# Optimization experiments

Measured on AMD Instinct MI355X. Metric: run time of the kernel, lower is better.

Reference implementation:

```python
import jax, jax.numpy as jnp
import numpy as np

DIM = 768
HID = 3072
HID2 = HID // 2
MAX_LEVEL = 8
N_LEV = MAX_LEVEL + 1
BATCH, SEQ = 2, 2048
EPS = 1e-5


def _layernorm(x, gamma, beta):
    m = jnp.mean(x, axis=-1, keepdims=True)
    v = jnp.mean(jnp.square(x - m), axis=-1, keepdims=True)
    return (x - m) * jax.lax.rsqrt(v + EPS) * gamma + beta


def setup_inputs() -> dict:
    key = jax.random.key(0)
    ks = jax.random.split(key, 12)
    s = 0.02
    return {
        "x": jax.random.normal(ks[0], (BATCH, SEQ, DIM), dtype=jnp.float32),
        "levels_info": jax.random.randint(ks[1], (SEQ, 4), 0, N_LEV, dtype=jnp.int32),
        "gamma": jnp.ones((DIM,), dtype=jnp.float32),
        "beta": jnp.zeros((DIM,), dtype=jnp.float32),
        "W1": jax.random.normal(ks[2], (DIM, HID), dtype=jnp.float32) * s,
        "b1": jnp.zeros((HID,), dtype=jnp.float32),
        "W2": jax.random.normal(ks[3], (HID, DIM), dtype=jnp.float32) * s,
        "b2": jnp.zeros((DIM,), dtype=jnp.float32),
        "A1": jax.random.normal(ks[4], (N_LEV, DIM, HID2), dtype=jnp.float32) * s,
        "a1b": jnp.zeros((N_LEV, HID2), dtype=jnp.float32),
        "A2": jax.random.normal(ks[5], (N_LEV, HID2, DIM), dtype=jnp.float32) * s,
        "a2b": jnp.zeros((N_LEV, DIM), dtype=jnp.float32),
        "lmw": jnp.ones((N_LEV,), dtype=jnp.float32)
        + jax.random.normal(ks[6], (N_LEV,), dtype=jnp.float32) * 0.1,
    }


def reference(x, levels_info, gamma, beta, W1, b1, W2, b2, A1, a1b, A2, a2b, lmw):
    # x: [B,S,D]
    x_norm = _layernorm(x, gamma, beta)
    # main MLP: Linear -> GELU (exact, torch default) -> Linear; dropout=0 is identity
    h = jax.nn.gelu(jnp.einsum("bsd,dh->bsh", x_norm, W1) + b1, approximate=False)
    main_out = jnp.einsum("bsh,hd->bsd", h, W2) + b2

    # per-token depth-indexed adapter routing
    depths = jnp.clip(levels_info[:, 0], 0, MAX_LEVEL)  # [S]
    level_adapted = jnp.zeros_like(main_out)
    for lvl in range(N_LEV):  # small fixed expert set
        mask = (depths == lvl).astype(x.dtype)[None, :, None]  # [1,S,1]
        hl = jax.nn.relu(jnp.einsum("bsd,dh->bsh", x_norm, A1[lvl]) + a1b[lvl])
        level_adapted = level_adapted + mask * (
            jnp.einsum("bsh,hd->bsd", hl, A2[lvl]) + a2b[lvl]
        )

    # softmax over the sequence axis (faithful to F.softmax(..., dim=0))
    mix = jax.nn.softmax(lmw[depths], axis=0)[None, :, None]  # [1,S,1]
    return main_out * (1.0 - mix) + level_adapted * mix
```

## Files before the change

### kernel.cpp

```cpp
#include <hip/hip_runtime.h>
#include <hip/hip_bf16.h>
#include <math.h>

typedef __bf16 bf16;
typedef __bf16 bf16x4 __attribute__((ext_vector_type(4)));
typedef __bf16 bf16x8 __attribute__((ext_vector_type(8)));
typedef float f32x4 __attribute__((ext_vector_type(4)));

#define DIM 768
#define HID 3072
#define HID2 1536
#define NLEV 9
#define SEQ 2048
#define ROWS 4096
#define MAXPAD 5248
#define MAXTILES 41

__device__ __forceinline__ void gld16(const void* g, void* l) {
    __builtin_amdgcn_global_load_lds(
        (const __attribute__((address_space(1))) void*)g,
        (__attribute__((address_space(3))) void*)l, 16, 0, 0);
}

__device__ __forceinline__ float fast_gelu(float v) {
    float v2 = v * v;
    float twou = v * (1.59576912f + 0.071354816f * v2);
    float t = __expf(twou);
    return v * t / (t + 1.0f);
}

__device__ __forceinline__ int xcd_swizzle(int s, int nwg) {
    int q = nwg >> 3, r = nwg & 7;
    int x = s & 7, i = s >> 3;
    return (x < r ? x * (q + 1) : r * (q + 1) + (x - r) * q) + i;
}


__device__ __forceinline__ void ln4_body(int blk,
                                         const float* __restrict__ x,
                                         const float* __restrict__ gamma,
                                         const float* __restrict__ beta,
                                         bf16* __restrict__ xn) {
    int tid = threadIdx.x;
    int wv = tid >> 6, ln = tid & 63;
    int row = blk * 4 + wv;
    const float* xr = x + (size_t)row * DIM;
    int c = ln * 4;
    float4 v0 = *(const float4*)(xr + c);
    float4 v1 = *(const float4*)(xr + c + 256);
    float4 v2 = *(const float4*)(xr + c + 512);
    float s = v0.x + v0.y + v0.z + v0.w
            + v1.x + v1.y + v1.z + v1.w
            + v2.x + v2.y + v2.z + v2.w;
    float q = v0.x * v0.x + v0.y * v0.y + v0.z * v0.z + v0.w * v0.w
            + v1.x * v1.x + v1.y * v1.y + v1.z * v1.z + v1.w * v1.w
            + v2.x * v2.x + v2.y * v2.y + v2.z * v2.z + v2.w * v2.w;
#pragma unroll
    for (int off = 32; off; off >>= 1) {
        s += __shfl_xor(s, off, 64);
        q += __shfl_xor(q, off, 64);
    }
    float m = s * (1.0f / DIM);
    float r = rsqrtf(q * (1.0f / DIM) - m * m + 1e-5f);
    bf16* xo = xn + (size_t)row * DIM;
#pragma unroll
    for (int p = 0; p < 3; p++) {
        int cc = c + p * 256;
        float4 v = (p == 0) ? v0 : (p == 1) ? v1 : v2;
        float4 g = *(const float4*)(gamma + cc);
        float4 b = *(const float4*)(beta + cc);
        bf16x4 o;
        o[0] = (bf16)((v.x - m) * r * g.x + b.x);
        o[1] = (bf16)((v.y - m) * r * g.y + b.y);
        o[2] = (bf16)((v.z - m) * r * g.z + b.z);
        o[3] = (bf16)((v.w - m) * r * g.w + b.w);
        *(bf16x4*)(xo + cc) = o;
    }
}

__device__ __forceinline__ void transpose_body64(bf16* sm,
                                                 const float* __restrict__ inb,
                                                 bf16* __restrict__ outb,
                                                 int R, int C, int bx, int by) {
    int tid = threadIdx.x;
    int ty = tid >> 4;
    int tx4 = (tid & 15) * 4;
#pragma unroll
    for (int p = 0; p < 4; p++) {
        int rloc = p * 16 + ty;
        int row = by * 64 + rloc;
        float4 v = *(const float4*)(inb + (size_t)row * C + bx * 64 + tx4);
        bf16x4 o;
        o[0] = (bf16)v.x; o[1] = (bf16)v.y; o[2] = (bf16)v.z; o[3] = (bf16)v.w;
        *(bf16x4*)(sm + rloc * 68 + tx4) = o;
    }
    __syncthreads();
    int ch = tid & 7;
    int ocb = tid >> 3;
#pragma unroll
    for (int p = 0; p < 2; p++) {
        int oc = p * 32 + ocb;
        bf16x8 tmp;
#pragma unroll
        for (int k = 0; k < 8; k++) tmp[k] = sm[(ch * 8 + k) * 68 + oc];
        *(bf16x8*)(outb + (size_t)(bx * 64 + oc) * R + by * 64 + ch * 8) = tmp;
    }
}

__device__ __forceinline__ void routing_body(float* sm,
                                             const int* __restrict__ levels_info,
                                             const float* __restrict__ lmw,
                                             float* __restrict__ mix,
                                             int* __restrict__ row_index,
                                             int* __restrict__ tile_meta,
                                             float* __restrict__ zbuf) {
    int* cnt = (int*)sm;
    int* cur = cnt + NLEV;
    int* off = cur + NLEV;
    float* mixv = (float*)(off + NLEV);
    int tid = threadIdx.x;
    if (tid < NLEV) { cnt[tid] = 0; cur[tid] = 0; }
    __syncthreads();
    for (int s = tid; s < SEQ; s += 256) {
        int d = levels_info[s * 4];
        d = d < 0 ? 0 : (d > 8 ? 8 : d);
        atomicAdd(&cnt[d], 1);
    }
    for (int i = tid; i < MAXPAD; i += 256) row_index[i] = -1;
    for (int i = tid; i < 1024; i += 256) zbuf[i] = 0.0f;
    __syncthreads();
    if (tid == 0) {
        float mx = lmw[0];
        for (int l = 1; l < NLEV; l++) mx = fmaxf(mx, lmw[l]);
        float denom = 0.f;
        for (int l = 0; l < NLEV; l++) denom += (float)cnt[l] * expf(lmw[l] - mx);
        float inv = 1.0f / denom;
        int running = 0, t = 0;
        for (int l = 0; l < NLEV; l++) {
            mixv[l] = expf(lmw[l] - mx) * inv;
            off[l] = running;
            int seg = (2 * cnt[l] + 127) & ~127;
            for (int k = 0; k < seg / 128; k++) tile_meta[t++] = l;
            running += seg;
        }
        for (; t < MAXTILES; t++) tile_meta[t] = -1;
    }
    __syncthreads();
    for (int s = tid; s < SEQ; s += 256) {
        int d = levels_info[s * 4];
        d = d < 0 ? 0 : (d > 8 ? 8 : d);
        int p = atomicAdd(&cur[d], 2);
        row_index[off[d] + p]     = s;
        row_index[off[d] + p + 1] = s + SEQ;
        mix[s] = mixv[d];
    }
}

__global__ __launch_bounds__(256) void prep_kernel(const float* __restrict__ x,
                                                   const int* __restrict__ levels_info,
                                                   const float* __restrict__ gamma,
                                                   const float* __restrict__ beta,
                                                   const float* __restrict__ W1,
                                                   const float* __restrict__ A1,
                                                   const float* __restrict__ W2,
                                                   const float* __restrict__ A2,
                                                   const float* __restrict__ lmw,
                                                   bf16* __restrict__ Xn,
                                                   bf16* __restrict__ W1t,
                                                   bf16* __restrict__ A1t,
                                                   bf16* __restrict__ W2t,
                                                   bf16* __restrict__ A2t,
                                                   float* __restrict__ mix,
                                                   int* __restrict__ row_index,
                                                   int* __restrict__ tile_meta,
                                                   float* __restrict__ zbuf) {
    __shared__ __align__(16) bf16 tsm[64 * 68];
    int b = blockIdx.x;
    if (b == 0) { routing_body((float*)tsm, levels_info, lmw, mix, row_index, tile_meta, zbuf); return; }
    b -= 1;
    if (b < 1024) { ln4_body(b, x, gamma, beta, Xn); return; }
    b -= 1024;
    if (b < 576) {
        transpose_body64(tsm, W1, W1t, DIM, HID, b % 48, b / 48);
        return;
    }
    b -= 576;
    if (b < 2592) {
        int bz = b / 288, r = b % 288;
        transpose_body64(tsm, A1 + (size_t)bz * DIM * HID2, A1t + (size_t)bz * DIM * HID2,
                         DIM, HID2, r % 24, r / 24);
        return;
    }
    b -= 2592;
    if (b < 576) {
        transpose_body64(tsm, W2, W2t, HID, DIM, b % 12, b / 12);
        return;
    }
    b -= 576;
    {
        int bz = b / 288, r = b % 288;
        transpose_body64(tsm, A2 + (size_t)bz * HID2 * DIM, A2t + (size_t)bz * HID2 * DIM,
                         HID2, DIM, r % 12, r / 12);
    }
}

template<int KT>
__device__ __forceinline__ void gemm_loop_db64(const bf16* (&ga)[4], const bf16* (&gb)[4],
                                               bf16* As, bf16* Bs,
                                               f32x4 (&acc)[4][4]) {
    int tid = threadIdx.x;
    int wv = tid >> 6;
    int lane = tid & 63;
    int wm = wv >> 1, wn = wv & 1;
    int r = lane & 15;
    int ch0 = ((lane >> 4) ^ (lane & 7)) * 8;
    int aoff = (wm * 64 + r) * 64 + ch0;
    int boff = (wn * 64 + r) * 64 + ch0;
#pragma unroll
    for (int c = 0; c < 4; c++) {
        gld16(ga[c], As + (c * 32 + wv * 8) * 64);
        gld16(gb[c], Bs + (c * 32 + wv * 8) * 64);
        ga[c] += 64; gb[c] += 64;
    }
#pragma unroll
    for (int kt = 0; kt < KT; ++kt) {
        __syncthreads();
        const int cur = (kt & 1) << 13;
        const int nxt = cur ^ 8192;
        if (kt + 1 < KT) {
#pragma unroll
            for (int c = 0; c < 4; c++) {
                gld16(ga[c], As + nxt + (c * 32 + wv * 8) * 64);
                gld16(gb[c], Bs + nxt + (c * 32 + wv * 8) * 64);
                ga[c] += 64; gb[c] += 64;
            }
        }
#pragma unroll
        for (int k32 = 0; k32 < 2; k32++) {
            const int kx = k32 << 5;
            bf16x8 af[4], bfr[4];
#pragma unroll
            for (int i = 0; i < 4; i++) af[i] = *(const bf16x8*)(As + cur + ((aoff + i * 1024) ^ kx));
#pragma unroll
            for (int j = 0; j < 4; j++) bfr[j] = *(const bf16x8*)(Bs + cur + ((boff + j * 1024) ^ kx));
#pragma unroll
            for (int i = 0; i < 4; i++)
#pragma unroll
                for (int j = 0; j < 4; j++)
                    acc[i][j] = __builtin_amdgcn_mfma_f32_16x16x32_bf16(af[i], bfr[j], acc[i][j], 0, 0, 0);
        }
    }
}

#define ACC_INIT(acc) \
    _Pragma("unroll") for (int i = 0; i < 4; i++) \
    _Pragma("unroll") for (int j = 0; j < 4; j++) acc[i][j] = (f32x4){0.f, 0.f, 0.f, 0.f};

__device__ __forceinline__ void store_tile(const bf16* cbuf, int lane,
                                           bf16* gptr, int ldg) {
#pragma unroll
    for (int p = 0; p < 8; p++) {
        int lrow = p * 8 + (lane >> 3);
        int chunk = (lane & 7) * 8;
        bf16x8 v = *(const bf16x8*)(cbuf + lrow * 64 + chunk);
        *(bf16x8*)(gptr + (size_t)lrow * ldg + chunk) = v;
    }
}

__global__ __launch_bounds__(256) void mlp1_kernel(const bf16* __restrict__ Xn,
                                                   const bf16* __restrict__ W1t,
                                                   const float* __restrict__ b1,
                                                   bf16* __restrict__ H,
                                                   const bf16* __restrict__ A1t,
                                                   const float* __restrict__ a1b,
                                                   const int* __restrict__ row_index,
                                                   const int* __restrict__ tile_meta,
                                                   const bf16* __restrict__ zbuf,
                                                   bf16* __restrict__ HL) {
    __shared__ __align__(16) bf16 smem[32768];
    bf16* As = smem;
    bf16* Bs = smem + 16384;
    int bid = xcd_swizzle(blockIdx.x, 1260);
    int tid = threadIdx.x;
    int lane = tid & 63, wv = tid >> 6, wm = wv >> 1, wn = wv & 1;
    int lrow = lane >> 3;
    int lch = ((lane & 7) ^ lrow) * 8;
    bf16* cbuf = smem + wv * 4096;

    if (bid < 768) {
        int s = bid >> 5, u = bid & 31;
        int nb = (s % 6) * 4 + (u & 3);
        int mb = (s / 6) * 8 + (u >> 2);
        f32x4 acc[4][4];
        ACC_INIT(acc);
        const bf16* ga[4]; const bf16* gb[4];
#pragma unroll
        for (int c = 0; c < 4; c++) {
            int rt = c * 32 + wv * 8 + lrow;
            ga[c] = Xn  + (size_t)(mb * 128 + rt) * DIM + lch;
            gb[c] = W1t + (size_t)(nb * 128 + rt) * DIM + lch;
        }
        gemm_loop_db64<12>(ga, gb, As, Bs, acc);
        int cbase = nb * 128 + wn * 64 + (lane & 15);
        __syncthreads();
#pragma unroll
        for (int j = 0; j < 4; j++) {
            float bias = b1[cbase + j * 16];
#pragma unroll
            for (int i = 0; i < 4; i++)
#pragma unroll
                for (int r = 0; r < 4; r++) {
                    int lr = i * 16 + ((lane >> 4) << 2) + r;
                    int lc = j * 16 + (lane & 15);
                    cbuf[lr * 64 + lc] = (bf16)fast_gelu(acc[i][j][r] + bias);
                }
        }
        __syncthreads();
        store_tile(cbuf, lane, H + (size_t)(mb * 128 + wm * 64) * HID + nb * 128 + wn * 64, HID);
    } else {
        int t2 = bid - 768;
        int nb = t2 % 12, t = t2 / 12;
        int lvl = tile_meta[t];
        if (lvl < 0) return;
        f32x4 acc[4][4];
        ACC_INIT(acc);
        const bf16* ga[4]; const bf16* gb[4];
        const bf16* Bl = A1t + (size_t)lvl * HID2 * DIM;
#pragma unroll
        for (int c = 0; c < 4; c++) {
            int rt = c * 32 + wv * 8 + lrow;
            int rg = row_index[t * 128 + rt];
            ga[c] = (rg >= 0) ? (Xn + (size_t)rg * DIM + lch) : (zbuf + lch);
            gb[c] = Bl + (size_t)(nb * 128 + rt) * DIM + lch;
        }
        gemm_loop_db64<12>(ga, gb, As, Bs, acc);
        int cbase = nb * 128 + wn * 64 + (lane & 15);
        __syncthreads();
#pragma unroll
        for (int j = 0; j < 4; j++) {
            float bias = a1b[lvl * HID2 + cbase + j * 16];
#pragma unroll
            for (int i = 0; i < 4; i++)
#pragma unroll
                for (int r = 0; r < 4; r++) {
                    int lr = i * 16 + ((lane >> 4) << 2) + r;
                    int lc = j * 16 + (lane & 15);
                    cbuf[lr * 64 + lc] = (bf16)fmaxf(acc[i][j][r] + bias, 0.0f);
                }
        }
        __syncthreads();
        store_tile(cbuf, lane, HL + (size_t)(t * 128 + wm * 64) * HID2 + nb * 128 + wn * 64, HID2);
    }
}

__global__ __launch_bounds__(256) void mlp2_kernel(const bf16* __restrict__ H,
                                                   const bf16* __restrict__ W2t,
                                                   bf16* __restrict__ part,
                                                   const bf16* __restrict__ HL,
                                                   const bf16* __restrict__ A2t,
                                                   const float* __restrict__ a2b,
                                                   const int* __restrict__ row_index,
                                                   const int* __restrict__ tile_meta,
                                                   bf16* __restrict__ apart) {
    __shared__ __align__(16) bf16 smem[32768];
    bf16* As = smem;
    bf16* Bs = smem + 16384;
    int bid = xcd_swizzle(blockIdx.x, 384 + MAXTILES * 6);
    int tid = threadIdx.x;
    int lane = tid & 63, wv = tid >> 6, wm = wv >> 1, wn = wv & 1;
    int lrow = lane >> 3;
    int lch = ((lane & 7) ^ lrow) * 8;
    bf16* cbuf = smem + wv * 4096;
    f32x4 acc[4][4];
    ACC_INIT(acc);

    if (bid < 384) {
        int cc = bid % 12;
        int nb = cc >> 1, ks = cc & 1;
        int mb = bid / 12;
        const bf16* ga[4]; const bf16* gb[4];
#pragma unroll
        for (int c = 0; c < 4; c++) {
            int rt = c * 32 + wv * 8 + lrow;
            ga[c] = H   + (size_t)(mb * 128 + rt) * HID + ks * 1536 + lch;
            gb[c] = W2t + (size_t)(nb * 128 + rt) * HID + ks * 1536 + lch;
        }
        gemm_loop_db64<24>(ga, gb, As, Bs, acc);
        __syncthreads();
#pragma unroll
        for (int j = 0; j < 4; j++)
#pragma unroll
            for (int i = 0; i < 4; i++)
#pragma unroll
                for (int r = 0; r < 4; r++) {
                    int lr = i * 16 + ((lane >> 4) << 2) + r;
                    int lc = j * 16 + (lane & 15);
                    cbuf[lr * 64 + lc] = (bf16)acc[i][j][r];
                }
        __syncthreads();
        bf16* pk = part + (size_t)ks * ROWS * DIM;
        store_tile(cbuf, lane, pk + (size_t)(mb * 128 + wm * 64) * DIM + nb * 128 + wn * 64, DIM);
    } else {
        int t2 = bid - 384;
        int nb = t2 % 6, t = t2 / 6;
        int lvl = tile_meta[t];
        if (lvl < 0) return;
        const bf16* ga[4]; const bf16* gb[4];
        const bf16* Bl = A2t + (size_t)lvl * DIM * HID2;
#pragma unroll
        for (int c = 0; c < 4; c++) {
            int rt = c * 32 + wv * 8 + lrow;
            ga[c] = HL + (size_t)(t * 128 + rt) * HID2 + lch;
            gb[c] = Bl + (size_t)(nb * 128 + rt) * HID2 + lch;
        }
        gemm_loop_db64<24>(ga, gb, As, Bs, acc);
        int cbase = nb * 128 + wn * 64 + (lane & 15);
        __syncthreads();
#pragma unroll
        for (int j = 0; j < 4; j++) {
            float bias = a2b[lvl * DIM + cbase + j * 16];
#pragma unroll
            for (int i = 0; i < 4; i++)
#pragma unroll
                for (int r = 0; r < 4; r++) {
                    int lr = i * 16 + ((lane >> 4) << 2) + r;
                    int lc = j * 16 + (lane & 15);
                    cbuf[lr * 64 + lc] = (bf16)(acc[i][j][r] + bias);
                }
        }
        __syncthreads();
        int colg = nb * 128 + wn * 64;
#pragma unroll
        for (int p = 0; p < 8; p++) {
            int lr = p * 8 + (lane >> 3);
            int chunk = (lane & 7) * 8;
            int rg = row_index[t * 128 + wm * 64 + lr];
            if (rg >= 0) {
                bf16x8 v = *(const bf16x8*)(cbuf + lr * 64 + chunk);
                *(bf16x8*)(apart + (size_t)rg * DIM + colg + chunk) = v;
            }
        }
    }
}

__global__ __launch_bounds__(256) void combine_kernel(const bf16* __restrict__ part,
                                                      const bf16* __restrict__ apart,
                                                      const float* __restrict__ b2,
                                                      const float* __restrict__ mix,
                                                      float* __restrict__ out) {
    int i = blockIdx.x * 256 + threadIdx.x;
    int base = i * 4;
    int row = base / DIM;
    int c = base - row * DIM;
    float mx = mix[row & (SEQ - 1)];
    bf16x4 p0 = *(const bf16x4*)(part + base);
    bf16x4 p1 = *(const bf16x4*)(part + (size_t)ROWS * DIM + base);
    bf16x4 a0 = *(const bf16x4*)(apart + base);
    float4 o;
    float* po = &o.x;
#pragma unroll
    for (int k = 0; k < 4; k++) {
        float main_v = (float)p0[k] + (float)p1[k] + b2[c + k];
        po[k] = (1.0f - mx) * main_v + mx * (float)a0[k];
    }
    *(float4*)(out + base) = o;
}

extern "C" void kernel_launch(void* const* d_in, const int* in_sizes, int n_in,
                              void* d_out, int out_size, void* d_ws, size_t ws_size,
                              hipStream_t stream) {
    const float* x    = (const float*)d_in[0];
    const int* levels = (const int*)d_in[1];
    const float* gamma= (const float*)d_in[2];
    const float* beta = (const float*)d_in[3];
    const float* W1   = (const float*)d_in[4];
    const float* b1   = (const float*)d_in[5];
    const float* W2   = (const float*)d_in[6];
    const float* b2   = (const float*)d_in[7];
    const float* A1   = (const float*)d_in[8];
    const float* a1b  = (const float*)d_in[9];
    const float* A2   = (const float*)d_in[10];
    const float* a2b  = (const float*)d_in[11];
    const float* lmw  = (const float*)d_in[12];
    float* out = (float*)d_out;

    char* p = (char*)d_ws;
    auto alloc = [&](size_t bytes) {
        char* r = p;
        p += (bytes + 255) & ~(size_t)255;
        return r;
    };
    bf16* Xn   = (bf16*)alloc((size_t)ROWS * DIM * 2);
    bf16* W1t  = (bf16*)alloc((size_t)HID * DIM * 2);
    bf16* W2t  = (bf16*)alloc((size_t)DIM * HID * 2);
    bf16* A1t  = (bf16*)alloc((size_t)NLEV * HID2 * DIM * 2);
    bf16* A2t  = (bf16*)alloc((size_t)NLEV * DIM * HID2 * 2);
    bf16* H    = (bf16*)alloc((size_t)ROWS * HID * 2);
    bf16* HL   = (bf16*)alloc((size_t)MAXPAD * HID2 * 2);
    bf16* part = (bf16*)alloc((size_t)2 * ROWS * DIM * 2);
    bf16* apart= (bf16*)alloc((size_t)ROWS * DIM * 2);
    float* mix = (float*)alloc(SEQ * 4);
    int* row_index = (int*)alloc(MAXPAD * 4);
    int* tile_meta = (int*)alloc(MAXTILES * 4);
    float* zbuf    = (float*)alloc(4096);

    prep_kernel<<<dim3(1 + 1024 + 576 + 2592 + 576 + 2592), dim3(256), 0, stream>>>(
        x, levels, gamma, beta, W1, A1, W2, A2, lmw,
        Xn, W1t, A1t, W2t, A2t, mix, row_index, tile_meta, zbuf);

    mlp1_kernel<<<dim3(768 + 492), dim3(256), 0, stream>>>(
        Xn, W1t, b1, H, A1t, a1b, row_index, tile_meta, (const bf16*)zbuf, HL);

    mlp2_kernel<<<dim3(384 + MAXTILES * 6), dim3(256), 0, stream>>>(
        H, W2t, part, HL, A2t, a2b, row_index, tile_meta, apart);

    combine_kernel<<<dim3(ROWS * DIM / 1024), dim3(256), 0, stream>>>(
        part, apart, b2, mix, out);
}
```

Measured before the change: 259.2 us.

## Switch GEMMs to 256x256 tiles with 8 waves and interleaved prefetch

Both MLP GEMM kernels move from 128x128 tiles with 4 waves to 256x256 tiles with 8 waves (512 threads, 128KB dynamic LDS). Each wave now holds an 8x4 MFMA accumulator block, which raises arithmetic intensity per LDS load. The K loop is split into barriered phases that interleave global-to-LDS prefetch with MFMA work and raise wave priority around the MFMAs. Adapter level segments are padded to 256 rows and the main down-projection uses a 4-way split-K that combine now sums. Larger padding wastes adapter compute, and the grid shrinks to 342 blocks, which risks poor CU occupancy and tail imbalance.

```diff
diff --git a/kernel.cpp b/kernel.cpp
--- a/kernel.cpp
+++ b/kernel.cpp
@@ -13,8 +13,8 @@
 #define NLEV 9
 #define SEQ 2048
 #define ROWS 4096
-#define MAXPAD 5248
-#define MAXTILES 41
+#define MAXPAD2 6400
+#define MAXT2 25
 
 __device__ __forceinline__ void gld16(const void* g, void* l) {
     __builtin_amdgcn_global_load_lds(
@@ -126,7 +126,7 @@
         d = d < 0 ? 0 : (d > 8 ? 8 : d);
         atomicAdd(&cnt[d], 1);
     }
-    for (int i = tid; i < MAXPAD; i += 256) row_index[i] = -1;
+    for (int i = tid; i < MAXPAD2; i += 256) row_index[i] = -1;
     for (int i = tid; i < 1024; i += 256) zbuf[i] = 0.0f;
     __syncthreads();
     if (tid == 0) {
@@ -139,11 +139,11 @@
         for (int l = 0; l < NLEV; l++) {
             mixv[l] = expf(lmw[l] - mx) * inv;
             off[l] = running;
-            int seg = (2 * cnt[l] + 127) & ~127;
-            for (int k = 0; k < seg / 128; k++) tile_meta[t++] = l;
+            int seg = (2 * cnt[l] + 255) & ~255;
+            for (int k = 0; k < seg / 256; k++) tile_meta[t++] = l;
             running += seg;
         }
-        for (; t < MAXTILES; t++) tile_meta[t] = -1;
+        for (; t < MAXT2; t++) tile_meta[t] = -1;
     }
     __syncthreads();
     for (int s = tid; s < SEQ; s += 256) {
@@ -204,70 +204,102 @@
     }
 }
 
+#define SBUF 16384
+
 template<int KT>
-__device__ __forceinline__ void gemm_loop_db64(const bf16* (&ga)[4], const bf16* (&gb)[4],
-                                               bf16* As, bf16* Bs,
-                                               f32x4 (&acc)[4][4]) {
-    int tid = threadIdx.x;
-    int wv = tid >> 6;
-    int lane = tid & 63;
-    int wm = wv >> 1, wn = wv & 1;
-    int r = lane & 15;
-    int ch0 = ((lane >> 4) ^ (lane & 7)) * 8;
-    int aoff = (wm * 64 + r) * 64 + ch0;
-    int boff = (wn * 64 + r) * 64 + ch0;
+__device__ __forceinline__ void gemm_loop_8w(const bf16* (&ga)[4], const bf16* (&gb)[4],
+                                             bf16* smem, f32x4 (&acc)[8][4]) {
+    const int tid = threadIdx.x;
+    const int wv = tid >> 6, lane = tid & 63;
+    const int wm = wv >> 2, wn = wv & 3;
+    const int r = lane & 15;
+    const int ch0 = ((lane >> 4) ^ (lane & 7)) * 8;
+    const int aoff = (wm * 128 + r) * 64 + ch0;
+    const int boff = (wn * 64 + r) * 64 + ch0;
+    bf16* As = smem;
+    bf16* Bs = smem + 2 * SBUF;
+    const int sA = wv * 512;
 #pragma unroll
     for (int c = 0; c < 4; c++) {
-        gld16(ga[c], As + (c * 32 + wv * 8) * 64);
-        gld16(gb[c], Bs + (c * 32 + wv * 8) * 64);
+        gld16(ga[c], As + sA + c * 4096);
+        gld16(gb[c], Bs + sA + c * 4096);
         ga[c] += 64; gb[c] += 64;
     }
-#pragma unroll
+#pragma unroll 2
     for (int kt = 0; kt < KT; ++kt) {
-        __syncthreads();
-        const int cur = (kt & 1) << 13;
-        const int nxt = cur ^ 8192;
+        const int cur = (kt & 1) ? SBUF : 0;
+        const int nxt = cur ^ SBUF;
+        const bf16* Ac = As + cur;
+        const bf16* Bc = Bs + cur;
+        bf16x8 a[4], b[4];
+        asm volatile("s_waitcnt vmcnt(0)" ::: "memory");
+        __builtin_amdgcn_s_barrier();
+        __builtin_amdgcn_sched_barrier(0);
         if (kt + 1 < KT) {
-#pragma unroll
-            for (int c = 0; c < 4; c++) {
-                gld16(ga[c], As + nxt + (c * 32 + wv * 8) * 64);
-                gld16(gb[c], Bs + nxt + (c * 32 + wv * 8) * 64);
-                ga[c] += 64; gb[c] += 64;
-            }
-        }
-#pragma unroll
-        for (int k32 = 0; k32 < 2; k32++) {
-            const int kx = k32 << 5;
-            bf16x8 af[4], bfr[4];
-#pragma unroll
-            for (int i = 0; i < 4; i++) af[i] = *(const bf16x8*)(As + cur + ((aoff + i * 1024) ^ kx));
-#pragma unroll
-            for (int j = 0; j < 4; j++) bfr[j] = *(const bf16x8*)(Bs + cur + ((boff + j * 1024) ^ kx));
-#pragma unroll
-            for (int i = 0; i < 4; i++)
-#pragma unroll
-                for (int j = 0; j < 4; j++)
-                    acc[i][j] = __builtin_amdgcn_mfma_f32_16x16x32_bf16(af[i], bfr[j], acc[i][j], 0, 0, 0);
-        }
-    }
-}
-
-#define ACC_INIT(acc) \
-    _Pragma("unroll") for (int i = 0; i < 4; i++) \
+            gld16(ga[0], As + nxt + sA);
+            gld16(gb[0], Bs + nxt + sA);
+            gld16(ga[1], As + nxt + sA + 4096);
+            gld16(gb[1], Bs + nxt + sA + 4096);
+            ga[0] += 64; gb[0] += 64; ga[1] += 64; gb[1] += 64;
+        }
+#pragma unroll
+        for (int i = 0; i < 4; i++) a[i] = *(const bf16x8*)(Ac + aoff + i * 1024);
+#pragma unroll
+        for (int j = 0; j < 4; j++) b[j] = *(const bf16x8*)(Bc + boff + j * 1024);
+        __builtin_amdgcn_s_setprio(1);
+#pragma unroll
+        for (int i = 0; i < 4; i++)
+#pragma unroll
+            for (int j = 0; j < 4; j++)
+                acc[i][j] = __builtin_amdgcn_mfma_f32_16x16x32_bf16(a[i], b[j], acc[i][j], 0, 0, 0);
+        __builtin_amdgcn_s_setprio(0);
+        __builtin_amdgcn_s_barrier();
+        if (kt + 1 < KT) {
+            gld16(ga[2], As + nxt + sA + 8192);
+            gld16(gb[2], Bs + nxt + sA + 8192);
+            gld16(ga[3], As + nxt + sA + 12288);
+            gld16(gb[3], Bs + nxt + sA + 12288);
+            ga[2] += 64; gb[2] += 64; ga[3] += 64; gb[3] += 64;
+        }
+#pragma unroll
+        for (int i = 0; i < 4; i++) a[i] = *(const bf16x8*)(Ac + aoff + (4 + i) * 1024);
+        __builtin_amdgcn_s_setprio(1);
+#pragma unroll
+        for (int i = 0; i < 4; i++)
+#pragma unroll
+            for (int j = 0; j < 4; j++)
+                acc[4 + i][j] = __builtin_amdgcn_mfma_f32_16x16x32_bf16(a[i], b[j], acc[4 + i][j], 0, 0, 0);
+        __builtin_amdgcn_s_setprio(0);
+        __builtin_amdgcn_s_barrier();
+#pragma unroll
+        for (int i = 0; i < 4; i++) a[i] = *(const bf16x8*)(Ac + ((aoff + i * 1024) ^ 32));
+#pragma unroll
+        for (int j = 0; j < 4; j++) b[j] = *(const bf16x8*)(Bc + ((boff + j * 1024) ^ 32));
+        __builtin_amdgcn_s_setprio(1);
+#pragma unroll
+        for (int i = 0; i < 4; i++)
+#pragma unroll
+            for (int j = 0; j < 4; j++)
+                acc[i][j] = __builtin_amdgcn_mfma_f32_16x16x32_bf16(a[i], b[j], acc[i][j], 0, 0, 0);
+        __builtin_amdgcn_s_setprio(0);
+        __builtin_amdgcn_s_barrier();
+#pragma unroll
+        for (int i = 0; i < 4; i++) a[i] = *(const bf16x8*)(Ac + ((aoff + (4 + i) * 1024) ^ 32));
+        __builtin_amdgcn_s_setprio(1);
+#pragma unroll
+        for (int i = 0; i < 4; i++)
+#pragma unroll
+            for (int j = 0; j < 4; j++)
+                acc[4 + i][j] = __builtin_amdgcn_mfma_f32_16x16x32_bf16(a[i], b[j], acc[4 + i][j], 0, 0, 0);
+        __builtin_amdgcn_s_setprio(0);
+    }
+}
+
+#define ACC_INIT8(acc) \
+    _Pragma("unroll") for (int i = 0; i < 8; i++) \
     _Pragma("unroll") for (int j = 0; j < 4; j++) acc[i][j] = (f32x4){0.f, 0.f, 0.f, 0.f};
 
-__device__ __forceinline__ void store_tile(const bf16* cbuf, int lane,
-                                           bf16* gptr, int ldg) {
-#pragma unroll
-    for (int p = 0; p < 8; p++) {
-        int lrow = p * 8 + (lane >> 3);
-        int chunk = (lane & 7) * 8;
-        bf16x8 v = *(const bf16x8*)(cbuf + lrow * 64 + chunk);
-        *(bf16x8*)(gptr + (size_t)lrow * ldg + chunk) = v;
-    }
-}
-
-__global__ __launch_bounds__(256) void mlp1_kernel(const bf16* __restrict__ Xn,
+__global__ __launch_bounds__(512) void mlp1_kernel(const bf16* __restrict__ Xn,
                                                    const bf16* __restrict__ W1t,
                                                    const float* __restrict__ b1,
                                                    bf16* __restrict__ H,
@@ -277,83 +309,86 @@
                                                    const int* __restrict__ tile_meta,
                                                    const bf16* __restrict__ zbuf,
                                                    bf16* __restrict__ HL) {
-    __shared__ __align__(16) bf16 smem[32768];
-    bf16* As = smem;
-    bf16* Bs = smem + 16384;
-    int bid = xcd_swizzle(blockIdx.x, 1260);
+    extern __shared__ __align__(16) bf16 smem[];
+    int bid = xcd_swizzle(blockIdx.x, 342);
     int tid = threadIdx.x;
-    int lane = tid & 63, wv = tid >> 6, wm = wv >> 1, wn = wv & 1;
-    int lrow = lane >> 3;
-    int lch = ((lane & 7) ^ lrow) * 8;
-    bf16* cbuf = smem + wv * 4096;
-
-    if (bid < 768) {
-        int s = bid >> 5, u = bid & 31;
-        int nb = (s % 6) * 4 + (u & 3);
-        int mb = (s / 6) * 8 + (u >> 2);
-        f32x4 acc[4][4];
-        ACC_INIT(acc);
+    int wv = tid >> 6, lane = tid & 63;
+    int wm = wv >> 2, wn = wv & 3;
+    int srow = lane >> 3;
+    int lch = ((lane & 7) ^ srow) * 8;
+    f32x4 acc[8][4];
+    ACC_INIT8(acc);
+    bf16* cbuf = smem + wv * 8192;
+
+    if (bid < 192) {
+        int nb = bid % 12, mb = bid / 12;
         const bf16* ga[4]; const bf16* gb[4];
 #pragma unroll
         for (int c = 0; c < 4; c++) {
-            int rt = c * 32 + wv * 8 + lrow;
-            ga[c] = Xn  + (size_t)(mb * 128 + rt) * DIM + lch;
-            gb[c] = W1t + (size_t)(nb * 128 + rt) * DIM + lch;
-        }
-        gemm_loop_db64<12>(ga, gb, As, Bs, acc);
-        int cbase = nb * 128 + wn * 64 + (lane & 15);
+            int rt = c * 64 + wv * 8 + srow;
+            ga[c] = Xn  + (size_t)(mb * 256 + rt) * DIM + lch;
+            gb[c] = W1t + (size_t)(nb * 256 + rt) * DIM + lch;
+        }
+        gemm_loop_8w<12>(ga, gb, smem, acc);
         __syncthreads();
+        int cbase = nb * 256 + wn * 64 + (lane & 15);
 #pragma unroll
         for (int j = 0; j < 4; j++) {
             float bias = b1[cbase + j * 16];
 #pragma unroll
-            for (int i = 0; i < 4; i++)
-#pragma unroll
-                for (int r = 0; r < 4; r++) {
-                    int lr = i * 16 + ((lane >> 4) << 2) + r;
-                    int lc = j * 16 + (lane & 15);
-                    cbuf[lr * 64 + lc] = (bf16)fast_gelu(acc[i][j][r] + bias);
+            for (int i = 0; i < 8; i++)
+#pragma unroll
+                for (int rr = 0; rr < 4; rr++) {
+                    int lr = i * 16 + ((lane >> 4) << 2) + rr;
+                    cbuf[lr * 64 + j * 16 + (lane & 15)] = (bf16)fast_gelu(acc[i][j][rr] + bias);
                 }
         }
-        __syncthreads();
-        store_tile(cbuf, lane, H + (size_t)(mb * 128 + wm * 64) * HID + nb * 128 + wn * 64, HID);
+        bf16* gp = H + (size_t)(mb * 256 + wm * 128) * HID + nb * 256 + wn * 64;
+#pragma unroll
+        for (int p = 0; p < 16; p++) {
+            int lr = p * 8 + srow;
+            int chunk = (lane & 7) * 8;
+            *(bf16x8*)(gp + (size_t)lr * HID + chunk) = *(const bf16x8*)(cbuf + lr * 64 + chunk);
+        }
     } else {
-        int t2 = bid - 768;
-        int nb = t2 % 12, t = t2 / 12;
+        int t2 = bid - 192;
+        int nb = t2 % 6, t = t2 / 6;
         int lvl = tile_meta[t];
         if (lvl < 0) return;
-        f32x4 acc[4][4];
-        ACC_INIT(acc);
         const bf16* ga[4]; const bf16* gb[4];
         const bf16* Bl = A1t + (size_t)lvl * HID2 * DIM;
 #pragma unroll
         for (int c = 0; c < 4; c++) {
-            int rt = c * 32 + wv * 8 + lrow;
-            int rg = row_index[t * 128 + rt];
+            int rt = c * 64 + wv * 8 + srow;
+            int rg = row_index[t * 256 + rt];
             ga[c] = (rg >= 0) ? (Xn + (size_t)rg * DIM + lch) : (zbuf + lch);
-            gb[c] = Bl + (size_t)(nb * 128 + rt) * DIM + lch;
-        }
-        gemm_loop_db64<12>(ga, gb, As, Bs, acc);
-        int cbase = nb * 128 + wn * 64 + (lane & 15);
+            gb[c] = Bl + (size_t)(nb * 256 + rt) * DIM + lch;
+        }
+        gemm_loop_8w<12>(ga, gb, smem, acc);
         __syncthreads();
+        int cbase = nb * 256 + wn * 64 + (lane & 15);
 #pragma unroll
         for (int j = 0; j < 4; j++) {
             float bias = a1b[lvl * HID2 + cbase + j * 16];
 #pragma unroll
-            for (int i = 0; i < 4; i++)
-#pragma unroll
-                for (int r = 0; r < 4; r++) {
-                    int lr = i * 16 + ((lane >> 4) << 2) + r;
-                    int lc = j * 16 + (lane & 15);
-                    cbuf[lr * 64 + lc] = (bf16)fmaxf(acc[i][j][r] + bias, 0.0f);
+            for (int i = 0; i < 8; i++)
+#pragma unroll
+                for (int rr = 0; rr < 4; rr++) {
+                    int lr = i * 16 + ((lane >> 4) << 2) + rr;
+                    cbuf[lr * 64 + j * 16 + (lane & 15)] = (bf16)fmaxf(acc[i][j][rr] + bias, 0.0f);
                 }
         }
-        __syncthreads();
-        store_tile(cbuf, lane, HL + (size_t)(t * 128 + wm * 64) * HID2 + nb * 128 + wn * 64, HID2);
-    }
-}
-
-__global__ __launch_bounds__(256) void mlp2_kernel(const bf16* __restrict__ H,
+        bf16* gp = HL + (size_t)(t * 256 + wm * 128) * HID2 + nb * 256 + wn * 64;
+#pragma unroll
+        for (int p = 0; p < 16; p++) {
+            int lr = p * 8 + srow;
+            int chunk = (lane & 7) * 8;
+            *(bf16x8*)(gp + (size_t)lr * HID2 + chunk) = *(const bf16x8*)(cbuf + lr * 64 + chunk);
+        }
+    }
+}
+
+__global__ __launch_bounds__(512) void mlp2_kernel(const bf16* __restrict__ H,
                                                    const bf16* __restrict__ W2t,
                                                    bf16* __restrict__ part,
                                                    const bf16* __restrict__ HL,
@@ -362,83 +397,84 @@
                                                    const int* __restrict__ row_index,
                                                    const int* __restrict__ tile_meta,
                                                    bf16* __restrict__ apart) {
-    __shared__ __align__(16) bf16 smem[32768];
-    bf16* As = smem;
-    bf16* Bs = smem + 16384;
-    int bid = xcd_swizzle(blockIdx.x, 384 + MAXTILES * 6);
+    extern __shared__ __align__(16) bf16 smem[];
+    int bid = xcd_swizzle(blockIdx.x, 342);
     int tid = threadIdx.x;
-    int lane = tid & 63, wv = tid >> 6, wm = wv >> 1, wn = wv & 1;
-    int lrow = lane >> 3;
-    int lch = ((lane & 7) ^ lrow) * 8;
-    bf16* cbuf = smem + wv * 4096;
-    f32x4 acc[4][4];
-    ACC_INIT(acc);
-
-    if (bid < 384) {
-        int cc = bid % 12;
-        int nb = cc >> 1, ks = cc & 1;
-        int mb = bid / 12;
-        const bf16* ga[4]; const bf16* gb[4];
-#pragma unroll
-        for (int c = 0; c < 4; c++) {
-            int rt = c * 32 + wv * 8 + lrow;
-            ga[c] = H   + (size_t)(mb * 128 + rt) * HID + ks * 1536 + lch;
-            gb[c] = W2t + (size_t)(nb * 128 + rt) * HID + ks * 1536 + lch;
-        }
-        gemm_loop_db64<24>(ga, gb, As, Bs, acc);
-        __syncthreads();
-#pragma unroll
-        for (int j = 0; j < 4; j++)
-#pragma unroll
-            for (int i = 0; i < 4; i++)
-#pragma unroll
-                for (int r = 0; r < 4; r++) {
-                    int lr = i * 16 + ((lane >> 4) << 2) + r;
-                    int lc = j * 16 + (lane & 15);
-                    cbuf[lr * 64 + lc] = (bf16)acc[i][j][r];
-                }
-        __syncthreads();
-        bf16* pk = part + (size_t)ks * ROWS * DIM;
-        store_tile(cbuf, lane, pk + (size_t)(mb * 128 + wm * 64) * DIM + nb * 128 + wn * 64, DIM);
-    } else {
-        int t2 = bid - 384;
-        int nb = t2 % 6, t = t2 / 6;
+    int wv = tid >> 6, lane = tid & 63;
+    int wm = wv >> 2, wn = wv & 3;
+    int srow = lane >> 3;
+    int lch = ((lane & 7) ^ srow) * 8;
+    f32x4 acc[8][4];
+    ACC_INIT8(acc);
+    bf16* cbuf = smem + wv * 8192;
+
+    if (bid < 150) {
+        int nb = bid % 3, t = bid / 3;
         int lvl = tile_meta[t];
         if (lvl < 0) return;
         const bf16* ga[4]; const bf16* gb[4];
         const bf16* Bl = A2t + (size_t)lvl * DIM * HID2;
 #pragma unroll
         for (int c = 0; c < 4; c++) {
-            int rt = c * 32 + wv * 8 + lrow;
-            ga[c] = HL + (size_t)(t * 128 + rt) * HID2 + lch;
-            gb[c] = Bl + (size_t)(nb * 128 + rt) * HID2 + lch;
-        }
-        gemm_loop_db64<24>(ga, gb, As, Bs, acc);
-        int cbase = nb * 128 + wn * 64 + (lane & 15);
+            int rt = c * 64 + wv * 8 + srow;
+            ga[c] = HL + (size_t)(t * 256 + rt) * HID2 + lch;
+            gb[c] = Bl + (size_t)(nb * 256 + rt) * HID2 + lch;
+        }
+        gemm_loop_8w<24>(ga, gb, smem, acc);
         __syncthreads();
+        int cbase = nb * 256 + wn * 64 + (lane & 15);
 #pragma unroll
         for (int j = 0; j < 4; j++) {
             float bias = a2b[lvl * DIM + cbase + j * 16];
 #pragma unroll
-            for (int i = 0; i < 4; i++)
-#pragma unroll
-                for (int r = 0; r < 4; r++) {
-                    int lr = i * 16 + ((lane >> 4) << 2) + r;
-                    int lc = j * 16 + (lane & 15);
-                    cbuf[lr * 64 + lc] = (bf16)(acc[i][j][r] + bias);
+            for (int i = 0; i < 8; i++)
+#pragma unroll
+                for (int rr = 0; rr < 4; rr++) {
+                    int lr = i * 16 + ((lane >> 4) << 2) + rr;
+                    cbuf[lr * 64 + j * 16 + (lane & 15)] = (bf16)(acc[i][j][rr] + bias);
                 }
         }
+        int colg = nb * 256 + wn * 64;
+#pragma unroll
+        for (int p = 0; p < 16; p++) {
+            int lr = p * 8 + srow;
+            int chunk = (lane & 7) * 8;
+            int rg = row_index[t * 256 + wm * 128 + lr];
+            if (rg >= 0) {
+                *(bf16x8*)(apart + (size_t)rg * DIM + colg + chunk) =
+                    *(const bf16x8*)(cbuf + lr * 64 + chunk);
+            }
+        }
+    } else {
+        int g = bid - 150;
+        int mb = g / 12;
+        int cc = g % 12;
+        int nb = cc >> 2, ks = cc & 3;
+        const bf16* ga[4]; const bf16* gb[4];
+#pragma unroll
+        for (int c = 0; c < 4; c++) {
+            int rt = c * 64 + wv * 8 + srow;
+            ga[c] = H   + (size_t)(mb * 256 + rt) * HID + ks * 768 + lch;
+            gb[c] = W2t + (size_t)(nb * 256 + rt) * HID + ks * 768 + lch;
+        }
+        gemm_loop_8w<12>(ga, gb, smem, acc);
         __syncthreads();
-        int colg = nb * 128 + wn * 64;
-#pragma unroll
-        for (int p = 0; p < 8; p++) {
-            int lr = p * 8 + (lane >> 3);
+#pragma unroll
+        for (int j = 0; j < 4; j++)
+#pragma unroll
+            for (int i = 0; i < 8; i++)
+#pragma unroll
+                for (int rr = 0; rr < 4; rr++) {
+                    int lr = i * 16 + ((lane >> 4) << 2) + rr;
+                    cbuf[lr * 64 + j * 16 + (lane & 15)] = (bf16)acc[i][j][rr];
+                }
+        bf16* gp = part + (size_t)ks * ROWS * DIM
+                 + (size_t)(mb * 256 + wm * 128) * DIM + nb * 256 + wn * 64;
+#pragma unroll
+        for (int p = 0; p < 16; p++) {
+            int lr = p * 8 + srow;
             int chunk = (lane & 7) * 8;
-            int rg = row_index[t * 128 + wm * 64 + lr];
-            if (rg >= 0) {
-                bf16x8 v = *(const bf16x8*)(cbuf + lr * 64 + chunk);
-                *(bf16x8*)(apart + (size_t)rg * DIM + colg + chunk) = v;
-            }
+            *(bf16x8*)(gp + (size_t)lr * DIM + chunk) = *(const bf16x8*)(cbuf + lr * 64 + chunk);
         }
     }
 }
@@ -455,12 +491,14 @@
     float mx = mix[row & (SEQ - 1)];
     bf16x4 p0 = *(const bf16x4*)(part + base);
     bf16x4 p1 = *(const bf16x4*)(part + (size_t)ROWS * DIM + base);
+    bf16x4 p2 = *(const bf16x4*)(part + (size_t)2 * ROWS * DIM + base);
+    bf16x4 p3 = *(const bf16x4*)(part + (size_t)3 * ROWS * DIM + base);
     bf16x4 a0 = *(const bf16x4*)(apart + base);
     float4 o;
     float* po = &o.x;
 #pragma unroll
     for (int k = 0; k < 4; k++) {
-        float main_v = (float)p0[k] + (float)p1[k] + b2[c + k];
+        float main_v = (float)p0[k] + (float)p1[k] + (float)p2[k] + (float)p3[k] + b2[c + k];
         po[k] = (1.0f - mx) * main_v + mx * (float)a0[k];
     }
     *(float4*)(out + base) = o;
@@ -496,22 +534,22 @@
     bf16* A1t  = (bf16*)alloc((size_t)NLEV * HID2 * DIM * 2);
     bf16* A2t  = (bf16*)alloc((size_t)NLEV * DIM * HID2 * 2);
     bf16* H    = (bf16*)alloc((size_t)ROWS * HID * 2);
-    bf16* HL   = (bf16*)alloc((size_t)MAXPAD * HID2 * 2);
-    bf16* part = (bf16*)alloc((size_t)2 * ROWS * DIM * 2);
+    bf16* HL   = (bf16*)alloc((size_t)MAXPAD2 * HID2 * 2);
+    bf16* part = (bf16*)alloc((size_t)4 * ROWS * DIM * 2);
     bf16* apart= (bf16*)alloc((size_t)ROWS * DIM * 2);
     float* mix = (float*)alloc(SEQ * 4);
-    int* row_index = (int*)alloc(MAXPAD * 4);
-    int* tile_meta = (int*)alloc(MAXTILES * 4);
+    int* row_index = (int*)alloc(MAXPAD2 * 4);
+    int* tile_meta = (int*)alloc(32 * 4);
     float* zbuf    = (float*)alloc(4096);
 
     prep_kernel<<<dim3(1 + 1024 + 576 + 2592 + 576 + 2592), dim3(256), 0, stream>>>(
         x, levels, gamma, beta, W1, A1, W2, A2, lmw,
         Xn, W1t, A1t, W2t, A2t, mix, row_index, tile_meta, zbuf);
 
-    mlp1_kernel<<<dim3(768 + 492), dim3(256), 0, stream>>>(
+    mlp1_kernel<<<dim3(342), dim3(512), 131072, stream>>>(
         Xn, W1t, b1, H, A1t, a1b, row_index, tile_meta, (const bf16*)zbuf, HL);
 
-    mlp2_kernel<<<dim3(384 + MAXTILES * 6), dim3(256), 0, stream>>>(
+    mlp2_kernel<<<dim3(342), dim3(512), 131072, stream>>>(
         H, W2t, part, HL, A2t, a2b, row_index, tile_meta, apart);
 
     combine_kernel<<<dim3(ROWS * DIM / 1024), dim3(256), 0, stream>>>(
```

Result: slower. 312.0 us (+20.3%).
